# Performance work log

Hardware: AMD Instinct MI355X
Metric: run time of the kernel (lower is better)

## Reference

```python
import jax, jax.numpy as jnp
import numpy as np

H = 16
D_MODEL = 1024
D_K = D_MODEL // H


def setup_inputs() -> dict:
    key = jax.random.key(0)
    ks = jax.random.split(key, 11)
    B, S = 2, 2048
    scale = 1.0 / np.sqrt(D_MODEL)
    inp = {
        "query": jax.random.normal(ks[0], (B, S, D_MODEL), dtype=jnp.float32),
        "key": jax.random.normal(ks[1], (B, S, D_MODEL), dtype=jnp.float32),
        "value": jax.random.normal(ks[2], (B, S, D_MODEL), dtype=jnp.float32),
        "Wq": jax.random.normal(ks[3], (D_MODEL, D_MODEL), dtype=jnp.float32) * scale,
        "bq": jnp.zeros((D_MODEL,), dtype=jnp.float32),
        "Wk": jax.random.normal(ks[4], (D_MODEL, D_MODEL), dtype=jnp.float32) * scale,
        "bk": jnp.zeros((D_MODEL,), dtype=jnp.float32),
        "Wv": jax.random.normal(ks[5], (D_MODEL, D_MODEL), dtype=jnp.float32) * scale,
        "bv": jnp.zeros((D_MODEL,), dtype=jnp.float32),
        "Wo": jax.random.normal(ks[6], (D_MODEL, D_MODEL), dtype=jnp.float32) * scale,
        "bo": jnp.zeros((D_MODEL,), dtype=jnp.float32),
    }
    return inp


def _mha(query, key, value, Wq, bq, Wk, bk, Wv, bv, Wo, bo):
    B, S, _ = query.shape
    # linear projections (torch nn.Linear: x @ W.T + b)
    q = query @ Wq.T + bq
    k = key @ Wk.T + bk
    v = value @ Wv.T + bv
    # split heads: [B, S, D] -> [B, H, S, d_k]
    q = q.reshape(B, S, H, D_K).transpose(0, 2, 1, 3)
    k = k.reshape(B, S, H, D_K).transpose(0, 2, 1, 3)
    v = v.reshape(B, S, H, D_K).transpose(0, 2, 1, 3)
    # scaled dot-product attention with manual stable softmax
    scores = jnp.einsum("bhqd,bhkd->bhqk", q, k) / jnp.sqrt(jnp.float32(D_K))
    stable = scores - jnp.max(scores, axis=-1, keepdims=True)
    e = jnp.exp(stable)
    attn = e / jnp.sum(e, axis=-1, keepdims=True)
    ctx = jnp.einsum("bhqk,bhkd->bhqd", attn, v)
    # merge heads and final projection
    ctx = ctx.transpose(0, 2, 1, 3).reshape(B, S, H * D_K)
    return ctx @ Wo.T + bo


def reference(query, key, value, Wq, bq, Wk, bk, Wv, bv, Wo, bo):
    return _mha(query, key, value, Wq, bq, Wk, bk, Wv, bv, Wo, bo)
```

## Files before the change

### kernel.cpp

```cpp
#include <hip/hip_runtime.h>


#define S_LEN 2048
#define BATCH 2
#define DM    1024
#define NH    16
#define DKH   64
#define BS    (BATCH * S_LEN)

typedef _Float16 f16x8 __attribute__((ext_vector_type(8)));
typedef _Float16 f16x4 __attribute__((ext_vector_type(4)));
typedef _Float16 f16x2 __attribute__((ext_vector_type(2)));
typedef __fp16   h16x2 __attribute__((ext_vector_type(2)));
typedef float    f32x4 __attribute__((ext_vector_type(4)));
typedef float    f32x16 __attribute__((ext_vector_type(16)));

__device__ __forceinline__ f16x2 pk_f16(float a, float b) {
  h16x2 r = __builtin_amdgcn_cvt_pkrtz(a, b);
  return __builtin_bit_cast(f16x2, r);
}

__device__ __forceinline__ void gld16(const void* g, void* l) {
  __builtin_amdgcn_global_load_lds(
      (const __attribute__((address_space(1))) void*)g,
      (__attribute__((address_space(3))) void*)l, 16, 0, 0);
}

__device__ __forceinline__ float fast_exp2(float x) {
#if __has_builtin(__builtin_amdgcn_exp2f)
  return __builtin_amdgcn_exp2f(x);
#else
  return exp2f(x);
#endif
}

__device__ __forceinline__ int swap23(int x) {
  return (x & ~12) | ((x & 4) << 1) | ((x & 8) >> 1);
}

__global__ __launch_bounds__(256) void cvt_all(
    const float* __restrict__ q, const float* __restrict__ k, const float* __restrict__ v,
    const float* __restrict__ wq, const float* __restrict__ wk,
    const float* __restrict__ wv, const float* __restrict__ wo,
    _Float16* __restrict__ xq, _Float16* __restrict__ xk, _Float16* __restrict__ xv,
    _Float16* __restrict__ w16)
{
  const int y = blockIdx.y;
  const float* src; _Float16* dst; int n;
  if (y == 0)      { src = q;  dst = xq; n = BS * DM; }
  else if (y == 1) { src = k;  dst = xk; n = BS * DM; }
  else if (y == 2) { src = v;  dst = xv; n = BS * DM; }
  else {
    src = (y == 3) ? wq : ((y == 4) ? wk : ((y == 5) ? wv : wo));
    dst = w16 + (size_t)(y - 3) * (DM * DM);
    n = DM * DM;
  }
  int i0 = (blockIdx.x * 256 + threadIdx.x) * 4;
  if (i0 < n) {
    float4 f = *(const float4*)(src + i0);
    f16x2 lo = pk_f16(f.x, f.y);
    f16x2 hi = pk_f16(f.z, f.w);
    f16x4 hh; hh[0] = lo[0]; hh[1] = lo[1]; hh[2] = hi[0]; hh[3] = hi[1];
    *(f16x4*)(dst + i0) = hh;
  }
}

template <typename OUT_T, bool VT>
__device__ __forceinline__ void gemm_core(
    const _Float16* __restrict__ A, const _Float16* __restrict__ W,
    const float* __restrict__ bias, OUT_T* __restrict__ out, float oscale)
{
  const int tid  = threadIdx.x;
  const int l    = tid & 63;
  const int wv   = tid >> 6;
  const int c    = l & 15, quad = l >> 4;
  const int m0   = blockIdx.x * 128, n0 = blockIdx.y * 128;
  const int wm   = wv & 1, wn = wv >> 1;
  __shared__ _Float16 sA[128 * 64];
  __shared__ _Float16 sB[128 * 64];

  const _Float16* gA[4]; const _Float16* gB[4];
#pragma unroll
  for (int p = 0; p < 4; ++p) {
    int s = tid + p * 256, r = s >> 3, g = (s & 7) ^ (r & 7);
    gA[p] = A + (size_t)(m0 + r) * DM + g * 8;
    gB[p] = W + (size_t)(n0 + r) * DM + g * 8;
  }
  const int cx = c & 7;

  f32x4 acc[4][4] = {};
  for (int k0 = 0; k0 < DM; k0 += 64) {
    __syncthreads();
#pragma unroll
    for (int p = 0; p < 4; ++p) {
      gld16(gA[p] + k0, sA + (tid + p * 256) * 8);
      gld16(gB[p] + k0, sB + (tid + p * 256) * 8);
    }
    __syncthreads();
#pragma unroll
    for (int ks = 0; ks < 2; ++ks) {
      f16x8 af[4], bf[4];
#pragma unroll
      for (int i = 0; i < 4; ++i)
        af[i] = *(const f16x8*)&sA[(wm * 64 + i * 16 + c) * 64 + ((ks * 4 + quad) ^ cx) * 8];
#pragma unroll
      for (int j = 0; j < 4; ++j)
        bf[j] = *(const f16x8*)&sB[(wn * 64 + j * 16 + c) * 64 + ((ks * 4 + quad) ^ cx) * 8];
#pragma unroll
      for (int i = 0; i < 4; ++i)
#pragma unroll
        for (int j = 0; j < 4; ++j) {
          if constexpr (VT)
            acc[i][j] = __builtin_amdgcn_mfma_f32_16x16x32_f16(af[i], bf[j], acc[i][j], 0, 0, 0);
          else
            acc[j][i] = __builtin_amdgcn_mfma_f32_16x16x32_f16(bf[j], af[i], acc[j][i], 0, 0, 0);
        }
    }
  }
  if constexpr (VT) {
#pragma unroll
    for (int j = 0; j < 4; ++j) {
      int col = n0 + wn * 64 + j * 16 + c;
      float bb = bias[col];
      int hh = col >> 6, dd = col & 63;
#pragma unroll
      for (int i = 0; i < 4; ++i) {
        int row = m0 + wm * 64 + i * 16 + quad * 4;
        int bb2 = row >> 11, ss = row & (S_LEN - 1);
        _Float16* dst = (_Float16*)out + ((size_t)(bb2 * NH + hh) * DKH + dd) * S_LEN + ss;
        f16x4 v4;
#pragma unroll
        for (int r = 0; r < 4; ++r) v4[r] = (_Float16)((acc[i][j][r] + bb) * oscale);
        *(f16x4*)dst = v4;
      }
    }
  } else {
#pragma unroll
    for (int j = 0; j < 4; ++j) {
      const int nb = n0 + wn * 64 + j * 16 + quad * 4;
      const f32x4 bb = *(const f32x4*)(bias + nb);
#pragma unroll
      for (int i = 0; i < 4; ++i) {
        const int m = m0 + wm * 64 + i * 16 + c;
        if constexpr (__is_same(OUT_T, float)) {
          f32x4 v4;
#pragma unroll
          for (int r = 0; r < 4; ++r) v4[r] = (acc[j][i][r] + bb[r]) * oscale;
          *(f32x4*)((float*)out + (size_t)m * DM + nb) = v4;
        } else {
          f16x4 v4;
#pragma unroll
          for (int r = 0; r < 4; ++r) v4[r] = (_Float16)((acc[j][i][r] + bb[r]) * oscale);
          *(f16x4*)((_Float16*)out + (size_t)m * DM + nb) = v4;
        }
      }
    }
  }
}

#define SC_Q (0.125f * 1.44269504088896340736f)

__global__ __launch_bounds__(256) void proj3(
    const _Float16* __restrict__ xq, const _Float16* __restrict__ xk,
    const _Float16* __restrict__ xv, const _Float16* __restrict__ w16,
    const float* __restrict__ bq, const float* __restrict__ bk, const float* __restrict__ bv,
    _Float16* __restrict__ Q, _Float16* __restrict__ K, _Float16* __restrict__ Vt)
{
  const int z = blockIdx.z;
  if (z == 2) {
    gemm_core<_Float16, true>(xv, w16 + (size_t)2 * DM * DM, bv, Vt, 1.0f);
  } else if (z == 0) {
    gemm_core<_Float16, false>(xq, w16, bq, Q, SC_Q);
  } else {
    gemm_core<_Float16, false>(xk, w16 + (size_t)DM * DM, bk, K, 1.0f);
  }
}

__global__ __launch_bounds__(256) void out_gemm(
    const _Float16* __restrict__ ctx, const _Float16* __restrict__ wo,
    const float* __restrict__ bo, float* __restrict__ out)
{
  gemm_core<float, false>(ctx, wo, bo, out, 1.0f);
}

__global__ __launch_bounds__(256, 2) void attn(
    const _Float16* __restrict__ Q, const _Float16* __restrict__ K,
    const _Float16* __restrict__ Vt, _Float16* __restrict__ ctx)
{
  const int tid = threadIdx.x;
  const int l   = tid & 63, wv = tid >> 6;
  const int lo5 = l & 31, hf = l >> 5;
  const int wq  = wv >> 1, wk = wv & 1;
  const int bh  = blockIdx.x;
  const int q0  = blockIdx.y * 128;
  const int b   = bh >> 4, hd = bh & 15;
  __shared__ _Float16 sK[2][64 * 64];
  __shared__ _Float16 sV[2][64 * 64];

  f16x8 qf0[4], qf1[4];
  {
    const _Float16* Qg0 = Q + ((size_t)(b * S_LEN + q0 + wq * 64 + lo5)) * DM + hd * DKH + 8 * hf;
    const _Float16* Qg1 = Qg0 + (size_t)32 * DM;
#pragma unroll
    for (int kc = 0; kc < 4; ++kc) { qf0[kc] = *(const f16x8*)(Qg0 + 16 * kc);
                                     qf1[kc] = *(const f16x8*)(Qg1 + 16 * kc); }
  }

  f32x16 o0[2] = {}, o1[2] = {};
  float l0 = 0.f, l1 = 0.f;
  const f16x2 ones = {(_Float16)1.0f, (_Float16)1.0f};

  const _Float16* Kg0 = K + ((size_t)b * S_LEN) * DM + hd * DKH;
  const _Float16* Vg0 = Vt + ((size_t)bh * DKH) * S_LEN;

  const int sa = tid,       ra = sa >> 3, ba = (sa & 7) ^ (ra & 7);
  const int sb = tid + 256, rb = sb >> 3, bb = (sb & 7) ^ (rb & 7);
  const _Float16* gKa = Kg0 + (size_t)swap23(ra) * DM + ba * 8;
  const _Float16* gKb = Kg0 + (size_t)swap23(rb) * DM + bb * 8;
  const _Float16* gVa = Vg0 + (size_t)ra * S_LEN + ba * 8;
  const _Float16* gVb = Vg0 + (size_t)rb * S_LEN + bb * 8;
  const int rx = lo5 & 7;

#define STAGE(t, bf) do {                                   \
    const size_t k0s = (size_t)(t) * 64;                    \
    gld16(gKa + k0s * DM, sK[bf] + sa * 8);                 \
    gld16(gKb + k0s * DM, sK[bf] + sb * 8);                 \
    gld16(gVa + k0s,      sV[bf] + sa * 8);                 \
    gld16(gVb + k0s,      sV[bf] + sb * 8);                 \
  } while (0)

  STAGE(0, 0);
  asm volatile("s_waitcnt vmcnt(0)" ::: "memory");
  __builtin_amdgcn_s_barrier();

  const int NT = S_LEN / 64;
  for (int kt = 0; kt < NT; ++kt) {
    const int cur = kt & 1;
    if (kt + 1 < NT) STAGE(kt + 1, cur ^ 1);

    const _Float16* sKc = sK[cur];
    const _Float16* sVc = sV[cur];

    f32x16 sA0 = {}, sA1 = {};
    __builtin_amdgcn_s_setprio(1);
#pragma unroll
    for (int kc = 0; kc < 4; ++kc) {
      f16x8 kf = *(const f16x8*)&sKc[(32 * wk + lo5) * 64 + ((2 * kc + hf) ^ rx) * 8];
      sA0 = __builtin_amdgcn_mfma_f32_32x32x16_f16(kf, qf0[kc], sA0, 0, 0, 0);
      sA1 = __builtin_amdgcn_mfma_f32_32x32x16_f16(kf, qf1[kc], sA1, 0, 0, 0);
    }
    __builtin_amdgcn_s_setprio(0);

    f16x8 p0[2], p1[2];
#pragma unroll
    for (int half = 0; half < 2; ++half)
#pragma unroll
      for (int j2 = 0; j2 < 4; ++j2) {
        float a0 = fast_exp2(sA0[8 * half + 2 * j2]);
        float a1 = fast_exp2(sA0[8 * half + 2 * j2 + 1]);
        f16x2 pka = pk_f16(a0, a1);
        p0[half][2 * j2]     = pka[0];
        p0[half][2 * j2 + 1] = pka[1];
        l0 = __builtin_amdgcn_fdot2(__builtin_bit_cast(h16x2, pka),
                                    __builtin_bit_cast(h16x2, ones), l0, false);
        float b0 = fast_exp2(sA1[8 * half + 2 * j2]);
        float b1 = fast_exp2(sA1[8 * half + 2 * j2 + 1]);
        f16x2 pkb = pk_f16(b0, b1);
        p1[half][2 * j2]     = pkb[0];
        p1[half][2 * j2 + 1] = pkb[1];
        l1 = __builtin_amdgcn_fdot2(__builtin_bit_cast(h16x2, pkb),
                                    __builtin_bit_cast(h16x2, ones), l1, false);
      }

    __builtin_amdgcn_s_setprio(1);
#pragma unroll
    for (int db = 0; db < 2; ++db)
#pragma unroll
      for (int half = 0; half < 2; ++half) {
        const int kc2 = 2 * wk + half;
        f16x8 vf = *(const f16x8*)&sVc[(32 * db + lo5) * 64 + ((2 * kc2 + hf) ^ rx) * 8];
        o0[db] = __builtin_amdgcn_mfma_f32_32x32x16_f16(p0[half], vf, o0[db], 0, 0, 0);
        o1[db] = __builtin_amdgcn_mfma_f32_32x32x16_f16(p1[half], vf, o1[db], 0, 0, 0);
      }
    __builtin_amdgcn_s_setprio(0);

    if (kt + 1 < NT) {
      asm volatile("s_waitcnt vmcnt(0)" ::: "memory");
      __builtin_amdgcn_s_barrier();
    }
  }
#undef STAGE

  __syncthreads();

  l0 += __shfl_xor(l0, 32);
  l1 += __shfl_xor(l1, 32);
  float* lbuf = (float*)&sV[0][0];
  float* obuf = (float*)&sK[0][0];
  if (hf == 0) {
    lbuf[((wq * 2 + 0) * 2 + wk) * 32 + lo5] = l0;
    lbuf[((wq * 2 + 1) * 2 + wk) * 32 + lo5] = l1;
  }
  __syncthreads();

  float inv0[16], inv1[16];
#pragma unroll
  for (int r = 0; r < 16; ++r) {
    int qq = 8 * (r >> 2) + 4 * hf + (r & 3);
    inv0[r] = 1.0f / (lbuf[((wq * 2 + 0) * 2 + 0) * 32 + qq] +
                      lbuf[((wq * 2 + 0) * 2 + 1) * 32 + qq]);
    inv1[r] = 1.0f / (lbuf[((wq * 2 + 1) * 2 + 0) * 32 + qq] +
                      lbuf[((wq * 2 + 1) * 2 + 1) * 32 + qq]);
  }

  _Float16* Og = ctx + ((size_t)(b * S_LEN + q0 + wq * 64)) * DM + hd * DKH;
#pragma unroll
  for (int db = 0; db < 2; ++db) {
    if (wk == 1) {
#pragma unroll
      for (int r = 0; r < 16; ++r) {
        int qq = 8 * (r >> 2) + 4 * hf + (r & 3);
        obuf[((wq * 2 + 0) * 32 + qq) * 32 + lo5] = o0[db][r];
        obuf[((wq * 2 + 1) * 32 + qq) * 32 + lo5] = o1[db][r];
      }
    }
    __syncthreads();
    if (wk == 0) {
#pragma unroll
      for (int r = 0; r < 16; ++r) {
        int qq = 8 * (r >> 2) + 4 * hf + (r & 3);
        float v0 = o0[db][r] + obuf[((wq * 2 + 0) * 32 + qq) * 32 + lo5];
        float v1 = o1[db][r] + obuf[((wq * 2 + 1) * 32 + qq) * 32 + lo5];
        Og[(size_t)qq * DM + 32 * db + lo5]        = (_Float16)(v0 * inv0[r]);
        Og[(size_t)(32 + qq) * DM + 32 * db + lo5] = (_Float16)(v1 * inv1[r]);
      }
    }
    __syncthreads();
  }
}

extern "C" void kernel_launch(void* const* d_in, const int* in_sizes, int n_in,
                              void* d_out, int out_size, void* d_ws, size_t ws_size,
                              hipStream_t stream)
{
  (void)in_sizes; (void)n_in; (void)out_size; (void)ws_size;
  const float* q  = (const float*)d_in[0];
  const float* k  = (const float*)d_in[1];
  const float* v  = (const float*)d_in[2];
  const float* wq = (const float*)d_in[3];
  const float* bq = (const float*)d_in[4];
  const float* wk = (const float*)d_in[5];
  const float* bk = (const float*)d_in[6];
  const float* wv = (const float*)d_in[7];
  const float* bv = (const float*)d_in[8];
  const float* wo = (const float*)d_in[9];
  const float* bo = (const float*)d_in[10];

  char* ws = (char*)d_ws;
  _Float16* XQ  = (_Float16*)(ws);
  _Float16* XK  = (_Float16*)(ws + (8u  << 20));
  _Float16* XV  = (_Float16*)(ws + (16u << 20));
  _Float16* W16 = (_Float16*)(ws + (24u << 20));
  _Float16* Qp  = (_Float16*)(ws + (32u << 20));
  _Float16* Kp  = (_Float16*)(ws + (40u << 20));
  _Float16* VT  = (_Float16*)(ws + (48u << 20));
  _Float16* CTX = XQ;
  float* out = (float*)d_out;

  cvt_all<<<dim3(4096, 7), 256, 0, stream>>>(q, k, v, wq, wk, wv, wo, XQ, XK, XV, W16);
  proj3<<<dim3(32, 8, 3), 256, 0, stream>>>(XQ, XK, XV, W16, bq, bk, bv, Qp, Kp, VT);
  attn<<<dim3(32, 16), 256, 0, stream>>>(Qp, Kp, VT, CTX);
  out_gemm<<<dim3(32, 8), 256, 0, stream>>>(CTX, W16 + (size_t)3 * DM * DM, bo, out);
}
```

Measured before the change: 226.2 us.

## Fuse fp32-to-fp16 conversion into projection GEMM tile loads

Removes the standalone conversion kernel and has the projection and output GEMMs load fp32 inputs and weights directly, converting to fp16 in registers before storing to LDS. This eliminates writing and rereading the fp16 copies of activations and weights, plus one kernel launch. In exchange, each GEMM block reads twice the bytes per tile from global memory, redundantly converts shared tiles across blocks, and loses the asynchronous global-to-LDS load path for fp32 operands.

New measurement: 242.9 us. 7.4% more time.

```diff
diff --git a/kernel.cpp b/kernel.cpp
--- a/kernel.cpp
+++ b/kernel.cpp
@@ -38,36 +38,20 @@
   return (x & ~12) | ((x & 4) << 1) | ((x & 8) >> 1);
 }
 
-__global__ __launch_bounds__(256) void cvt_all(
-    const float* __restrict__ q, const float* __restrict__ k, const float* __restrict__ v,
-    const float* __restrict__ wq, const float* __restrict__ wk,
-    const float* __restrict__ wv, const float* __restrict__ wo,
-    _Float16* __restrict__ xq, _Float16* __restrict__ xk, _Float16* __restrict__ xv,
-    _Float16* __restrict__ w16)
-{
-  const int y = blockIdx.y;
-  const float* src; _Float16* dst; int n;
-  if (y == 0)      { src = q;  dst = xq; n = BS * DM; }
-  else if (y == 1) { src = k;  dst = xk; n = BS * DM; }
-  else if (y == 2) { src = v;  dst = xv; n = BS * DM; }
-  else {
-    src = (y == 3) ? wq : ((y == 4) ? wk : ((y == 5) ? wv : wo));
-    dst = w16 + (size_t)(y - 3) * (DM * DM);
-    n = DM * DM;
-  }
-  int i0 = (blockIdx.x * 256 + threadIdx.x) * 4;
-  if (i0 < n) {
-    float4 f = *(const float4*)(src + i0);
-    f16x2 lo = pk_f16(f.x, f.y);
-    f16x2 hi = pk_f16(f.z, f.w);
-    f16x4 hh; hh[0] = lo[0]; hh[1] = lo[1]; hh[2] = hi[0]; hh[3] = hi[1];
-    *(f16x4*)(dst + i0) = hh;
-  }
-}
-
-template <typename OUT_T, bool VT>
+__device__ __forceinline__ f16x8 cvt8(const float* __restrict__ p) {
+  float4 x0 = *(const float4*)p;
+  float4 x1 = *(const float4*)(p + 4);
+  f16x2 c0 = pk_f16(x0.x, x0.y), c1 = pk_f16(x0.z, x0.w);
+  f16x2 c2 = pk_f16(x1.x, x1.y), c3 = pk_f16(x1.z, x1.w);
+  f16x8 h;
+  h[0] = c0[0]; h[1] = c0[1]; h[2] = c1[0]; h[3] = c1[1];
+  h[4] = c2[0]; h[5] = c2[1]; h[6] = c3[0]; h[7] = c3[1];
+  return h;
+}
+
+template <typename OUT_T, bool VT, bool A32, bool B32>
 __device__ __forceinline__ void gemm_core(
-    const _Float16* __restrict__ A, const _Float16* __restrict__ W,
+    const void* __restrict__ Av, const void* __restrict__ Wv,
     const float* __restrict__ bias, OUT_T* __restrict__ out, float oscale)
 {
   const int tid  = threadIdx.x;
@@ -79,22 +63,42 @@
   __shared__ _Float16 sA[128 * 64];
   __shared__ _Float16 sB[128 * 64];
 
-  const _Float16* gA[4]; const _Float16* gB[4];
+  const _Float16* gA16[4]; const float* gA32[4];
+  const _Float16* gB16[4]; const float* gB32[4];
 #pragma unroll
   for (int p = 0; p < 4; ++p) {
     int s = tid + p * 256, r = s >> 3, g = (s & 7) ^ (r & 7);
-    gA[p] = A + (size_t)(m0 + r) * DM + g * 8;
-    gB[p] = W + (size_t)(n0 + r) * DM + g * 8;
+    if constexpr (A32) gA32[p] = (const float*)Av + (size_t)(m0 + r) * DM + g * 8;
+    else               gA16[p] = (const _Float16*)Av + (size_t)(m0 + r) * DM + g * 8;
+    if constexpr (B32) gB32[p] = (const float*)Wv + (size_t)(n0 + r) * DM + g * 8;
+    else               gB16[p] = (const _Float16*)Wv + (size_t)(n0 + r) * DM + g * 8;
   }
   const int cx = c & 7;
 
   f32x4 acc[4][4] = {};
   for (int k0 = 0; k0 < DM; k0 += 64) {
     __syncthreads();
-#pragma unroll
-    for (int p = 0; p < 4; ++p) {
-      gld16(gA[p] + k0, sA + (tid + p * 256) * 8);
-      gld16(gB[p] + k0, sB + (tid + p * 256) * 8);
+    if constexpr (!A32) {
+#pragma unroll
+      for (int p = 0; p < 4; ++p) gld16(gA16[p] + k0, sA + (tid + p * 256) * 8);
+    }
+    if constexpr (!B32) {
+#pragma unroll
+      for (int p = 0; p < 4; ++p) gld16(gB16[p] + k0, sB + (tid + p * 256) * 8);
+    }
+    if constexpr (A32) {
+      f16x8 st[4];
+#pragma unroll
+      for (int p = 0; p < 4; ++p) st[p] = cvt8(gA32[p] + k0);
+#pragma unroll
+      for (int p = 0; p < 4; ++p) *(f16x8*)(sA + (tid + p * 256) * 8) = st[p];
+    }
+    if constexpr (B32) {
+      f16x8 st[4];
+#pragma unroll
+      for (int p = 0; p < 4; ++p) st[p] = cvt8(gB32[p] + k0);
+#pragma unroll
+      for (int p = 0; p < 4; ++p) *(f16x8*)(sB + (tid + p * 256) * 8) = st[p];
     }
     __syncthreads();
 #pragma unroll
@@ -161,26 +165,26 @@
 #define SC_Q (0.125f * 1.44269504088896340736f)
 
 __global__ __launch_bounds__(256) void proj3(
-    const _Float16* __restrict__ xq, const _Float16* __restrict__ xk,
-    const _Float16* __restrict__ xv, const _Float16* __restrict__ w16,
+    const float* __restrict__ xq, const float* __restrict__ xk, const float* __restrict__ xv,
+    const float* __restrict__ wqp, const float* __restrict__ wkp, const float* __restrict__ wvp,
     const float* __restrict__ bq, const float* __restrict__ bk, const float* __restrict__ bv,
     _Float16* __restrict__ Q, _Float16* __restrict__ K, _Float16* __restrict__ Vt)
 {
   const int z = blockIdx.z;
   if (z == 2) {
-    gemm_core<_Float16, true>(xv, w16 + (size_t)2 * DM * DM, bv, Vt, 1.0f);
+    gemm_core<_Float16, true, true, true>(xv, wvp, bv, Vt, 1.0f);
   } else if (z == 0) {
-    gemm_core<_Float16, false>(xq, w16, bq, Q, SC_Q);
+    gemm_core<_Float16, false, true, true>(xq, wqp, bq, Q, SC_Q);
   } else {
-    gemm_core<_Float16, false>(xk, w16 + (size_t)DM * DM, bk, K, 1.0f);
+    gemm_core<_Float16, false, true, true>(xk, wkp, bk, K, 1.0f);
   }
 }
 
 __global__ __launch_bounds__(256) void out_gemm(
-    const _Float16* __restrict__ ctx, const _Float16* __restrict__ wo,
+    const _Float16* __restrict__ ctx, const float* __restrict__ wo,
     const float* __restrict__ bo, float* __restrict__ out)
 {
-  gemm_core<float, false>(ctx, wo, bo, out, 1.0f);
+  gemm_core<float, false, false, true>(ctx, wo, bo, out, 1.0f);
 }
 
 __global__ __launch_bounds__(256, 2) void attn(
@@ -357,18 +361,13 @@
   const float* bo = (const float*)d_in[10];
 
   char* ws = (char*)d_ws;
-  _Float16* XQ  = (_Float16*)(ws);
-  _Float16* XK  = (_Float16*)(ws + (8u  << 20));
-  _Float16* XV  = (_Float16*)(ws + (16u << 20));
-  _Float16* W16 = (_Float16*)(ws + (24u << 20));
-  _Float16* Qp  = (_Float16*)(ws + (32u << 20));
-  _Float16* Kp  = (_Float16*)(ws + (40u << 20));
-  _Float16* VT  = (_Float16*)(ws + (48u << 20));
-  _Float16* CTX = XQ;
+  _Float16* CTX = (_Float16*)(ws);
+  _Float16* Qp  = (_Float16*)(ws + (8u  << 20));
+  _Float16* Kp  = (_Float16*)(ws + (16u << 20));
+  _Float16* VT  = (_Float16*)(ws + (24u << 20));
   float* out = (float*)d_out;
 
-  cvt_all<<<dim3(4096, 7), 256, 0, stream>>>(q, k, v, wq, wk, wv, wo, XQ, XK, XV, W16);
-  proj3<<<dim3(32, 8, 3), 256, 0, stream>>>(XQ, XK, XV, W16, bq, bk, bv, Qp, Kp, VT);
+  proj3<<<dim3(32, 8, 3), 256, 0, stream>>>(q, k, v, wq, wk, wv, bq, bk, bv, Qp, Kp, VT);
   attn<<<dim3(32, 16), 256, 0, stream>>>(Qp, Kp, VT, CTX);
-  out_gemm<<<dim3(32, 8), 256, 0, stream>>>(CTX, W16 + (size_t)3 * DM * DM, bo, out);
-}
+  out_gemm<<<dim3(32, 8), 256, 0, stream>>>(CTX, wo, bo, out);
+}
```
